# Optimization experiments

Measured on AMD Instinct MI355X. Metric: run time of the kernel, lower is better.

## Reference

```python
import jax, jax.numpy as jnp
import numpy as np

LN_EPS = 1e-5
BN_EPS = 1e-5
ALPHA = 0.1

def _layer_norm(x):
    # F.layer_norm over last dim, no affine
    mu = jnp.mean(x, axis=-1, keepdims=True)
    var = jnp.var(x, axis=-1, keepdims=True)
    return (x - mu) * jax.lax.rsqrt(var + LN_EPS)

def setup_inputs() -> dict:
    key = jax.random.key(0)
    ks = jax.random.split(key, 12)
    N, Nh, D, Dq = 8192, 8192, 64, 64
    s = 1.0 / np.sqrt(D)
    inp = {
        "X": jax.random.normal(ks[0], (N, D), jnp.float32),
        "H": jax.random.normal(ks[1], (Nh, D), jnp.float32),
        "M": jax.random.uniform(ks[2], (N, Nh), jnp.float32),
        # Linear params (torch nn.Linear: y = x @ W.T + b), uniform init scale
        "Qw": jax.random.uniform(ks[3], (Dq, D), jnp.float32, -s, s),
        "Qb": jax.random.uniform(ks[4], (Dq,), jnp.float32, -s, s),
        "Kw": jax.random.uniform(ks[5], (Dq, D), jnp.float32, -s, s),
        "Kb": jax.random.uniform(ks[6], (Dq,), jnp.float32, -s, s),
        "Vw": jax.random.uniform(ks[7], (64, D), jnp.float32, -s, s),
        "Vb": jax.random.uniform(ks[8], (64,), jnp.float32, -s, s),
        # BatchNorm1d(64) eval-mode params
        "bn_gamma": jnp.ones((64,), jnp.float32),
        "bn_beta": jnp.zeros((64,), jnp.float32),
        "bn_mean": 0.1 * jax.random.normal(ks[9], (64,), jnp.float32),
        "bn_var": jax.random.uniform(ks[10], (64,), jnp.float32, 0.5, 1.5),
    }
    return inp

def reference(X, H, M, Qw, Qb, Kw, Kb, Vw, Vb, bn_gamma, bn_beta, bn_mean, bn_var):
    # K/Q branches: Linear + LayerNorm
    K = _layer_norm(H @ Kw.T + Kb)            # [Nh, Dq]
    Q = _layer_norm(X @ Qw.T + Qb)            # [N, Dq]
    # V branch: Linear + BatchNorm1d (eval mode; dropout is identity in eval)
    V = (H @ Vw.T + Vb - bn_mean) * jax.lax.rsqrt(bn_var + BN_EPS) * bn_gamma + bn_beta  # [Nh, 64]
    # Masked attention, softmax over dim=0 (columns)
    A = (Q @ K.T) * 0.125                     # [N, Nh]
    A = jax.nn.softmax(M * A, axis=0)
    # globel=True branch
    return ALPHA * (A @ V) + M @ H            # [N, 64]
```

## Files before the change

kernel.cpp:

```cpp
#include <hip/hip_runtime.h>
#include <hip/hip_bf16.h>
#include <math.h>

#define NN 8192
#define QSCALE (0.125f * 1.44269504088896f)
#define OSZ (8192*64)

typedef __attribute__((ext_vector_type(8))) short short8;
typedef __attribute__((ext_vector_type(16))) float f32x16;
typedef __attribute__((ext_vector_type(4))) unsigned uint4e;
typedef __attribute__((ext_vector_type(2))) unsigned uint2e;

union W4 { uint4e u4; unsigned u[4]; short8 v; };

__device__ inline unsigned short f2bf(float x) {
  union { float f; unsigned u; } t; t.f = x;
  unsigned r = t.u + 0x7fffu + ((t.u >> 16) & 1u);
  return (unsigned short)(r >> 16);
}
__device__ inline unsigned cvtpk(float lo, float hi) {
  unsigned r;
  asm("v_cvt_pk_bf16_f32 %0, %1, %2" : "=v"(r) : "v"(lo), "v"(hi));
  return r;
}

__global__ __launch_bounds__(256) void qkv_kernel(
    const float* __restrict__ X, const float* __restrict__ H,
    const float* __restrict__ Qw, const float* __restrict__ Qb,
    const float* __restrict__ Kw, const float* __restrict__ Kb,
    const float* __restrict__ Vw, const float* __restrict__ Vb,
    const float* __restrict__ bng, const float* __restrict__ bnb,
    const float* __restrict__ bnm, const float* __restrict__ bnv,
    unsigned short* __restrict__ QP, unsigned short* __restrict__ KP,
    unsigned short* __restrict__ VP, unsigned short* __restrict__ HP)
{
  int wid = (blockIdx.x * blockDim.x + threadIdx.x) >> 6;
  int d = threadIdx.x & 63;
  float4 w[16];

  for (int fq = 0; fq < 16; fq++) w[fq] = *(const float4*)(Qw + d*64 + fq*4);
  for (int rr = 0; rr < 4; rr++) {
    int r = wid*4 + rr;
    float a = Qb[d];
    for (int fq = 0; fq < 16; fq++) {
      float4 xv = *(const float4*)(X + r*64 + fq*4);
      a += w[fq].x*xv.x + w[fq].y*xv.y + w[fq].z*xv.z + w[fq].w*xv.w;
    }
    float s = a;
    for (int off = 32; off; off >>= 1) s += __shfl_xor(s, off);
    float mean = s * (1.f/64.f);
    float c = a - mean;
    float s2 = c*c;
    for (int off = 32; off; off >>= 1) s2 += __shfl_xor(s2, off);
    float q = c * rsqrtf(s2*(1.f/64.f) + 1e-5f);
    QP[(d>>3)*65536 + r*8 + (d&7)] = f2bf(q * QSCALE);
  }
  for (int fq = 0; fq < 16; fq++) w[fq] = *(const float4*)(Kw + d*64 + fq*4);
  for (int rr = 0; rr < 4; rr++) {
    int r = wid*4 + rr;
    float a = Kb[d];
    for (int fq = 0; fq < 16; fq++) {
      float4 hv = *(const float4*)(H + r*64 + fq*4);
      a += w[fq].x*hv.x + w[fq].y*hv.y + w[fq].z*hv.z + w[fq].w*hv.w;
    }
    float s = a;
    for (int off = 32; off; off >>= 1) s += __shfl_xor(s, off);
    float mean = s * (1.f/64.f);
    float c = a - mean;
    float s2 = c*c;
    for (int off = 32; off; off >>= 1) s2 += __shfl_xor(s2, off);
    float k = c * rsqrtf(s2*(1.f/64.f) + 1e-5f);
    KP[(d>>3)*65536 + r*8 + (d&7)] = f2bf(k);
  }
  for (int fq = 0; fq < 16; fq++) w[fq] = *(const float4*)(Vw + d*64 + fq*4);
  float bscale = rsqrtf(bnv[d] + 1e-5f) * bng[d];
  for (int rr = 0; rr < 4; rr++) {
    int r = wid*4 + rr;
    float a = Vb[d];
    for (int fq = 0; fq < 16; fq++) {
      float4 hv = *(const float4*)(H + r*64 + fq*4);
      a += w[fq].x*hv.x + w[fq].y*hv.y + w[fq].z*hv.z + w[fq].w*hv.w;
    }
    float v = (a - bnm[d]) * bscale + bnb[d];
    VP[(r>>3)*512 + d*8 + (r&7)] = f2bf(v);
    HP[(r>>3)*512 + d*8 + (r&7)] = f2bf(H[r*64 + d]);
  }
}

__global__ __launch_bounds__(256) void pass1_kernel(
    const float* __restrict__ M, const unsigned short* __restrict__ QP,
    const unsigned short* __restrict__ KP, unsigned* __restrict__ MT4,
    float* __restrict__ pd)
{
  __shared__ __align__(16) float ld[4][32*34];
  int tid = threadIdx.x;
  int wj = (blockIdx.x * blockDim.x + tid) >> 6;
  int lane = tid & 63;
  int wv = tid >> 6;
  int l31 = lane & 31, h = lane >> 5;
  int jb = wj & 255, slice = wj >> 8;
  int j = jb*32 + l31;
  float* lds = ld[wv];

  short8 kb[4];
  for (int m = 0; m < 4; m++)
    kb[m] = *(const short8*)(KP + (2*m + h)*65536 + j*8);

  float d0 = 0.f, d1 = 0.f, d2 = 0.f, d3 = 0.f;
  for (int t = 0; t < 8; t++) {
    int i0 = (slice*8 + t) * 32;
    f32x16 acc;
    for (int r = 0; r < 16; r++) acc[r] = 0.f;
    for (int m = 0; m < 4; m++) {
      short8 qa = *(const short8*)(QP + (2*m + h)*65536 + (size_t)(i0 + l31)*8);
      acc = __builtin_amdgcn_mfma_f32_32x32x16_bf16(qa, kb[m], acc, 0, 0, 0);
    }
    float Mv[16];
#pragma unroll
    for (int r = 0; r < 16; r++) {
      int ir = (r&3) + 8*(r>>2) + 4*h;
      Mv[r] = __builtin_nontemporal_load(M + (size_t)(i0 + ir)*NN + j);
      lds[ir*34 + l31] = Mv[r];
    }
    d0 += exp2f(acc[0]*Mv[0]) + exp2f(acc[4]*Mv[4]) + exp2f(acc[8]*Mv[8])   + exp2f(acc[12]*Mv[12]);
    d1 += exp2f(acc[1]*Mv[1]) + exp2f(acc[5]*Mv[5]) + exp2f(acc[9]*Mv[9])   + exp2f(acc[13]*Mv[13]);
    d2 += exp2f(acc[2]*Mv[2]) + exp2f(acc[6]*Mv[6]) + exp2f(acc[10]*Mv[10]) + exp2f(acc[14]*Mv[14]);
    d3 += exp2f(acc[3]*Mv[3]) + exp2f(acc[7]*Mv[7]) + exp2f(acc[11]*Mv[11]) + exp2f(acc[15]*Mv[15]);

    asm volatile("s_waitcnt lgkmcnt(0)" ::: "memory");
    int ii = l31;
    int i_g = i0 + ii;
#pragma unroll
    for (int qq = 0; qq < 2; qq++) {
      int q = 2*h + qq;
      unsigned w0, w1, w2, w3;
      {
        float2 a2 = *(const float2*)(&lds[ii*34 + 8*q + 0]);
        float2 b2 = *(const float2*)(&lds[ii*34 + 8*q + 2]);
        float2 c2 = *(const float2*)(&lds[ii*34 + 8*q + 4]);
        float2 e2 = *(const float2*)(&lds[ii*34 + 8*q + 6]);
        w0 = cvtpk(a2.x, a2.y); w1 = cvtpk(b2.x, b2.y);
        w2 = cvtpk(c2.x, c2.y); w3 = cvtpk(e2.x, e2.y);
      }
      uint4e ww = {w0, w1, w2, w3};
      *(uint4e*)(MT4 + (size_t)(jb*4 + q)*32768 + (size_t)i_g*4) = ww;
    }
  }
  float drun = (d0 + d1) + (d2 + d3);
  drun += __shfl_xor(drun, 32);
  if (lane < 32) pd[(size_t)slice*NN + j] = drun;
}

__global__ __launch_bounds__(256) void combine_kernel(
    const float* __restrict__ pd, float* __restrict__ colcc)
{
  int j = blockIdx.x * blockDim.x + threadIdx.x;
  float Dv = 0.f;
  for (int s = 0; s < 32; s++) Dv += pd[(size_t)s*NN + j];
  colcc[j] = log2f(Dv * 10.f);
}

__global__ __launch_bounds__(256) void pass2_kernel(
    const unsigned* __restrict__ MT4, const unsigned short* __restrict__ QP,
    const unsigned short* __restrict__ KP, const unsigned short* __restrict__ VP,
    const unsigned short* __restrict__ HP, const float* __restrict__ colcc,
    float* __restrict__ opart)
{
  __shared__ __align__(16) float cls[512];

  int iblk = blockIdx.x >> 4, slice = blockIdx.x & 15;
  int i0 = iblk * 64;
  int tid = threadIdx.x;
  int lane = tid & 63, wid = tid >> 6;
  int l31 = lane & 31, h = lane >> 5;
  int iq = wid & 1, dh = wid >> 1;
  int row = iq*32 + l31;
  int i_g = i0 + row;

  short8 qb[4];
  for (int m = 0; m < 4; m++)
    qb[m] = *(const short8*)(QP + (2*m + h)*65536 + (size_t)i_g*8);

  cls[tid]       = colcc[slice*512 + tid];
  cls[tid + 256] = colcc[slice*512 + 256 + tid];
  __syncthreads();

  f32x16 oacc;
  for (int r = 0; r < 16; r++) oacc[r] = 0.f;

  const unsigned* mbase = MT4 + (size_t)i_g*4;

  for (int t = 0; t < 16; t++) {
    int jt = slice*512 + t*32;
    int jtb = jt >> 3;

    W4 A0, A1; uint2e E0, E1;
    A0.u4 = *(const uint4e*)(mbase + (size_t)(jtb + h)*32768);
    A1.u4 = *(const uint4e*)(mbase + (size_t)(jtb + 2 + h)*32768);
    E0    = *(const uint2e*)(mbase + (size_t)(jtb + (h ? 0 : 1))*32768 + 2*h);
    E1    = *(const uint2e*)(mbase + (size_t)(jtb + (h ? 2 : 3))*32768 + 2*h);

    f32x16 sacc;
    for (int r = 0; r < 16; r++) sacc[r] = 0.f;
    for (int m = 0; m < 4; m++) {
      short8 ka = *(const short8*)(KP + (2*m + h)*65536 + (size_t)(jt + l31)*8);
      sacc = __builtin_amdgcn_mfma_f32_32x32x16_bf16(ka, qb[m], sacc, 0, 0, 0);
    }

    unsigned mw[8];
    mw[0] = h ? E0.x    : A0.u[0];  mw[1] = h ? E0.y    : A0.u[1];
    mw[2] = h ? A0.u[2] : E0.x;     mw[3] = h ? A0.u[3] : E0.y;
    mw[4] = h ? E1.x    : A1.u[0];  mw[5] = h ? E1.y    : A1.u[1];
    mw[6] = h ? A1.u[2] : E1.x;     mw[7] = h ? A1.u[3] : E1.y;

    float p[16];
#pragma unroll
    for (int q = 0; q < 4; q++) {
      float4 cc = *(const float4*)(&cls[t*32 + 8*q + 4*h]);
      unsigned wa = mw[2*q], wb = mw[2*q + 1];
      float m0 = __uint_as_float(wa << 16);
      float m1 = __uint_as_float(wa & 0xffff0000u);
      float m2 = __uint_as_float(wb << 16);
      float m3 = __uint_as_float(wb & 0xffff0000u);
      p[4*q+0] = exp2f(fmaf(sacc[4*q+0], m0, -cc.x));
      p[4*q+1] = exp2f(fmaf(sacc[4*q+1], m1, -cc.y));
      p[4*q+2] = exp2f(fmaf(sacc[4*q+2], m2, -cc.z));
      p[4*q+3] = exp2f(fmaf(sacc[4*q+3], m3, -cc.w));
    }
    unsigned pu[8];
#pragma unroll
    for (int k = 0; k < 8; k++) pu[k] = cvtpk(p[2*k], p[2*k+1]);

    asm volatile("v_permlane32_swap_b32 %0, %1" : "+v"(pu[0]), "+v"(pu[2]));
    asm volatile("v_permlane32_swap_b32 %0, %1" : "+v"(pu[1]), "+v"(pu[3]));
    asm volatile("v_permlane32_swap_b32 %0, %1" : "+v"(pu[4]), "+v"(pu[6]));
    asm volatile("v_permlane32_swap_b32 %0, %1" : "+v"(pu[5]), "+v"(pu[7]));

    W4 PA0, PA1;
    PA0.u[0] = pu[0]; PA0.u[1] = pu[1]; PA0.u[2] = pu[2]; PA0.u[3] = pu[3];
    PA1.u[0] = pu[4]; PA1.u[1] = pu[5]; PA1.u[2] = pu[6]; PA1.u[3] = pu[7];

    int j8 = jt >> 3;
    const unsigned short* vbase = VP + (size_t)j8*512 + (dh*32 + l31)*8;
    const unsigned short* hbase = HP + (size_t)j8*512 + (dh*32 + l31)*8;
    short8 vb1 = *(const short8*)(vbase + h*512);
    short8 vb2 = *(const short8*)(vbase + (2 + h)*512);
    short8 hb1 = *(const short8*)(hbase + h*512);
    short8 hb2 = *(const short8*)(hbase + (2 + h)*512);

    oacc = __builtin_amdgcn_mfma_f32_32x32x16_bf16(PA0.v, vb1, oacc, 0, 0, 0);
    oacc = __builtin_amdgcn_mfma_f32_32x32x16_bf16(PA1.v, vb2, oacc, 0, 0, 0);
    oacc = __builtin_amdgcn_mfma_f32_32x32x16_bf16(A0.v,  hb1, oacc, 0, 0, 0);
    oacc = __builtin_amdgcn_mfma_f32_32x32x16_bf16(A1.v,  hb2, oacc, 0, 0, 0);
  }

  float* obase = opart + (size_t)slice*OSZ;
#pragma unroll
  for (int r = 0; r < 16; r++) {
    int orow = i0 + iq*32 + (r&3) + 8*(r>>2) + 4*h;
    int ocol = dh*32 + l31;
    obase[(size_t)orow*64 + ocol] = oacc[r];
  }
}

__global__ __launch_bounds__(256) void reduce_kernel(
    const float* __restrict__ opart, float* __restrict__ out)
{
  int e4 = blockIdx.x * blockDim.x + threadIdx.x;
  const float4* p = (const float4*)opart;
  float4 a = p[e4];
#pragma unroll
  for (int s = 1; s < 16; s++) {
    float4 b = p[(size_t)s*(OSZ/4) + e4];
    a.x += b.x; a.y += b.y; a.z += b.z; a.w += b.w;
  }
  ((float4*)out)[e4] = a;
}

extern "C" void kernel_launch(void* const* d_in, const int* in_sizes, int n_in,
                              void* d_out, int out_size, void* d_ws, size_t ws_size,
                              hipStream_t stream) {
  const float* X   = (const float*)d_in[0];
  const float* H   = (const float*)d_in[1];
  const float* M   = (const float*)d_in[2];
  const float* Qw  = (const float*)d_in[3];
  const float* Qb  = (const float*)d_in[4];
  const float* Kw  = (const float*)d_in[5];
  const float* Kb  = (const float*)d_in[6];
  const float* Vw  = (const float*)d_in[7];
  const float* Vb  = (const float*)d_in[8];
  const float* bng = (const float*)d_in[9];
  const float* bnb = (const float*)d_in[10];
  const float* bnm = (const float*)d_in[11];
  const float* bnv = (const float*)d_in[12];
  float* out = (float*)d_out;

  char* ws = (char*)d_ws;
  const size_t MB = 1024*1024;
  unsigned* MT4       = (unsigned*)(ws);
  unsigned short* QP  = (unsigned short*)(ws + 128*MB);
  unsigned short* KP  = (unsigned short*)(ws + 129*MB);
  unsigned short* VP  = (unsigned short*)(ws + 130*MB);
  unsigned short* HP  = (unsigned short*)(ws + 131*MB);
  float* pd           = (float*)(ws + 132*MB);
  float* colcc        = (float*)(ws + 133*MB);
  float* opart        = (float*)(ws + 134*MB);

  qkv_kernel<<<512, 256, 0, stream>>>(X, H, Qw, Qb, Kw, Kb, Vw, Vb,
                                      bng, bnb, bnm, bnv, QP, KP, VP, HP);
  pass1_kernel<<<2048, 256, 0, stream>>>(M, QP, KP, MT4, pd);
  combine_kernel<<<32, 256, 0, stream>>>(pd, colcc);
  pass2_kernel<<<2048, 256, 0, stream>>>(MT4, QP, KP, VP, HP, colcc, opart);
  reduce_kernel<<<512, 256, 0, stream>>>(opart, out);
}
```

Before: 200.7 us.

## Prefetch next-tile M and K loads; derive mask words via permlane swap

In pass1, the M tile for the next row block is loaded one iteration early into registers so its global load latency overlaps the current MFMA and exp work. In pass2, the next tile's transposed-mask words and K fragments are software-prefetched, and V/H fragment loads are moved to the top of the loop. The two extra uint2 mask loads are replaced by v_permlane32_swap on the already-loaded words. This costs extra registers, which could lower occupancy. There is also a leftover redundant assignment (A0c = A1n) that is immediately overwritten.

```diff
diff --git a/kernel.cpp b/kernel.cpp
--- a/kernel.cpp
+++ b/kernel.cpp
@@ -9,7 +9,6 @@
 typedef __attribute__((ext_vector_type(8))) short short8;
 typedef __attribute__((ext_vector_type(16))) float f32x16;
 typedef __attribute__((ext_vector_type(4))) unsigned uint4e;
-typedef __attribute__((ext_vector_type(2))) unsigned uint2e;
 
 union W4 { uint4e u4; unsigned u[4]; short8 v; };
 
@@ -106,20 +105,39 @@
   for (int m = 0; m < 4; m++)
     kb[m] = *(const short8*)(KP + (2*m + h)*65536 + j*8);
 
+  float Mv[16];
+  {
+    int i0 = slice*8*32;
+#pragma unroll
+    for (int r = 0; r < 16; r++) {
+      int ir = (r&3) + 8*(r>>2) + 4*h;
+      Mv[r] = __builtin_nontemporal_load(M + (size_t)(i0 + ir)*NN + j);
+    }
+  }
+
   float d0 = 0.f, d1 = 0.f, d2 = 0.f, d3 = 0.f;
   for (int t = 0; t < 8; t++) {
     int i0 = (slice*8 + t) * 32;
+    float Mn[16];
+    if (t < 7) {
+      int i1 = i0 + 32;
+#pragma unroll
+      for (int r = 0; r < 16; r++) {
+        int ir = (r&3) + 8*(r>>2) + 4*h;
+        Mn[r] = __builtin_nontemporal_load(M + (size_t)(i1 + ir)*NN + j);
+      }
+    }
+
     f32x16 acc;
     for (int r = 0; r < 16; r++) acc[r] = 0.f;
     for (int m = 0; m < 4; m++) {
       short8 qa = *(const short8*)(QP + (2*m + h)*65536 + (size_t)(i0 + l31)*8);
       acc = __builtin_amdgcn_mfma_f32_32x32x16_bf16(qa, kb[m], acc, 0, 0, 0);
     }
-    float Mv[16];
+
 #pragma unroll
     for (int r = 0; r < 16; r++) {
       int ir = (r&3) + 8*(r>>2) + 4*h;
-      Mv[r] = __builtin_nontemporal_load(M + (size_t)(i0 + ir)*NN + j);
       lds[ir*34 + l31] = Mv[r];
     }
     d0 += exp2f(acc[0]*Mv[0]) + exp2f(acc[4]*Mv[4]) + exp2f(acc[8]*Mv[8])   + exp2f(acc[12]*Mv[12]);
@@ -145,6 +163,10 @@
       uint4e ww = {w0, w1, w2, w3};
       *(uint4e*)(MT4 + (size_t)(jb*4 + q)*32768 + (size_t)i_g*4) = ww;
     }
+    if (t < 7) {
+#pragma unroll
+      for (int r = 0; r < 16; r++) Mv[r] = Mn[r];
+    }
   }
   float drun = (d0 + d1) + (d2 + d3);
   drun += __shfl_xor(drun, 32);
@@ -190,28 +212,49 @@
 
   const unsigned* mbase = MT4 + (size_t)i_g*4;
 
+  W4 A0c, A1c; short8 kac[4];
+  {
+    int jt = slice*512, jtb = jt >> 3;
+    A0c.u4 = *(const uint4e*)(mbase + (size_t)(jtb + h)*32768);
+    A1c.u4 = *(const uint4e*)(mbase + (size_t)(jtb + 2 + h)*32768);
+    for (int m = 0; m < 4; m++)
+      kac[m] = *(const short8*)(KP + (2*m + h)*65536 + (size_t)(jt + l31)*8);
+  }
+
   for (int t = 0; t < 16; t++) {
     int jt = slice*512 + t*32;
-    int jtb = jt >> 3;
-
-    W4 A0, A1; uint2e E0, E1;
-    A0.u4 = *(const uint4e*)(mbase + (size_t)(jtb + h)*32768);
-    A1.u4 = *(const uint4e*)(mbase + (size_t)(jtb + 2 + h)*32768);
-    E0    = *(const uint2e*)(mbase + (size_t)(jtb + (h ? 0 : 1))*32768 + 2*h);
-    E1    = *(const uint2e*)(mbase + (size_t)(jtb + (h ? 2 : 3))*32768 + 2*h);
+
+    W4 A0n, A1n; short8 kan[4];
+    if (t < 15) {
+      int jn = jt + 32, jnb = jn >> 3;
+      A0n.u4 = *(const uint4e*)(mbase + (size_t)(jnb + h)*32768);
+      A1n.u4 = *(const uint4e*)(mbase + (size_t)(jnb + 2 + h)*32768);
+      for (int m = 0; m < 4; m++)
+        kan[m] = *(const short8*)(KP + (2*m + h)*65536 + (size_t)(jn + l31)*8);
+    }
+
+    int j8 = jt >> 3;
+    const unsigned short* vbase = VP + (size_t)j8*512 + (dh*32 + l31)*8;
+    const unsigned short* hbase = HP + (size_t)j8*512 + (dh*32 + l31)*8;
+    short8 vb1 = *(const short8*)(vbase + h*512);
+    short8 vb2 = *(const short8*)(vbase + (2 + h)*512);
+    short8 hb1 = *(const short8*)(hbase + h*512);
+    short8 hb2 = *(const short8*)(hbase + (2 + h)*512);
 
     f32x16 sacc;
     for (int r = 0; r < 16; r++) sacc[r] = 0.f;
-    for (int m = 0; m < 4; m++) {
-      short8 ka = *(const short8*)(KP + (2*m + h)*65536 + (size_t)(jt + l31)*8);
-      sacc = __builtin_amdgcn_mfma_f32_32x32x16_bf16(ka, qb[m], sacc, 0, 0, 0);
-    }
-
-    unsigned mw[8];
-    mw[0] = h ? E0.x    : A0.u[0];  mw[1] = h ? E0.y    : A0.u[1];
-    mw[2] = h ? A0.u[2] : E0.x;     mw[3] = h ? A0.u[3] : E0.y;
-    mw[4] = h ? E1.x    : A1.u[0];  mw[5] = h ? E1.y    : A1.u[1];
-    mw[6] = h ? A1.u[2] : E1.x;     mw[7] = h ? A1.u[3] : E1.y;
+    for (int m = 0; m < 4; m++)
+      sacc = __builtin_amdgcn_mfma_f32_32x32x16_bf16(kac[m], qb[m], sacc, 0, 0, 0);
+
+    unsigned mw0 = A0c.u[0], mw2 = A0c.u[2];
+    unsigned mw1 = A0c.u[1], mw3 = A0c.u[3];
+    unsigned mw4 = A1c.u[0], mw6 = A1c.u[2];
+    unsigned mw5 = A1c.u[1], mw7 = A1c.u[3];
+    asm volatile("v_permlane32_swap_b32 %0, %1" : "+v"(mw0), "+v"(mw2));
+    asm volatile("v_permlane32_swap_b32 %0, %1" : "+v"(mw1), "+v"(mw3));
+    asm volatile("v_permlane32_swap_b32 %0, %1" : "+v"(mw4), "+v"(mw6));
+    asm volatile("v_permlane32_swap_b32 %0, %1" : "+v"(mw5), "+v"(mw7));
+    unsigned mw[8] = {mw0, mw1, mw2, mw3, mw4, mw5, mw6, mw7};
 
     float p[16];
 #pragma unroll
@@ -240,18 +283,18 @@
     PA0.u[0] = pu[0]; PA0.u[1] = pu[1]; PA0.u[2] = pu[2]; PA0.u[3] = pu[3];
     PA1.u[0] = pu[4]; PA1.u[1] = pu[5]; PA1.u[2] = pu[6]; PA1.u[3] = pu[7];
 
-    int j8 = jt >> 3;
-    const unsigned short* vbase = VP + (size_t)j8*512 + (dh*32 + l31)*8;
-    const unsigned short* hbase = HP + (size_t)j8*512 + (dh*32 + l31)*8;
-    short8 vb1 = *(const short8*)(vbase + h*512);
-    short8 vb2 = *(const short8*)(vbase + (2 + h)*512);
-    short8 hb1 = *(const short8*)(hbase + h*512);
-    short8 hb2 = *(const short8*)(hbase + (2 + h)*512);
-
     oacc = __builtin_amdgcn_mfma_f32_32x32x16_bf16(PA0.v, vb1, oacc, 0, 0, 0);
     oacc = __builtin_amdgcn_mfma_f32_32x32x16_bf16(PA1.v, vb2, oacc, 0, 0, 0);
-    oacc = __builtin_amdgcn_mfma_f32_32x32x16_bf16(A0.v,  hb1, oacc, 0, 0, 0);
-    oacc = __builtin_amdgcn_mfma_f32_32x32x16_bf16(A1.v,  hb2, oacc, 0, 0, 0);
+    oacc = __builtin_amdgcn_mfma_f32_32x32x16_bf16(A0c.v, hb1, oacc, 0, 0, 0);
+    oacc = __builtin_amdgcn_mfma_f32_32x32x16_bf16(A1c.v, hb2, oacc, 0, 0, 0);
+
+    if (t < 15) {
+      A0c = A1n;
+    }
+    if (t < 15) {
+      A0c = A0n; A1c = A1n;
+      for (int m = 0; m < 4; m++) kac[m] = kan[m];
+    }
   }
 
   float* obase = opart + (size_t)slice*OSZ;
```

Measured after the change: 200.8 us. No clear change (+0.1%).

## Drop bf16 transposed M copy; re-read fp32 M in pass2 via LDS

Applied to the files above, without the earlier changes.

Pass1 no longer writes a transposed bf16 copy of M (128MB workspace). It now only computes column denominators, prefetching the next M tile into registers and using raw v_exp_f32. Pass2 instead streams fp32 M directly through double-buffered LDS tiles, converting to bf16 in registers with permlane swaps, and uses 8 slices instead of 16, which halves the partial-output reduction. This trades a 128MB write plus 128MB bf16 read for a second 256MB fp32 read of M, and adds LDS traffic and per-tile barriers.

```diff
diff --git a/kernel.cpp b/kernel.cpp
--- a/kernel.cpp
+++ b/kernel.cpp
@@ -5,13 +5,12 @@
 #define NN 8192
 #define QSCALE (0.125f * 1.44269504088896f)
 #define OSZ (8192*64)
+#define NSL 8
 
 typedef __attribute__((ext_vector_type(8))) short short8;
 typedef __attribute__((ext_vector_type(16))) float f32x16;
-typedef __attribute__((ext_vector_type(4))) unsigned uint4e;
-typedef __attribute__((ext_vector_type(2))) unsigned uint2e;
-
-union W4 { uint4e u4; unsigned u[4]; short8 v; };
+
+union W4 { unsigned u[4]; short8 v; };
 
 __device__ inline unsigned short f2bf(float x) {
   union { float f; unsigned u; } t; t.f = x;
@@ -21,6 +20,11 @@
 __device__ inline unsigned cvtpk(float lo, float hi) {
   unsigned r;
   asm("v_cvt_pk_bf16_f32 %0, %1, %2" : "=v"(r) : "v"(lo), "v"(hi));
+  return r;
+}
+__device__ inline float fexp2(float x) {
+  float r;
+  asm("v_exp_f32 %0, %1" : "=v"(r) : "v"(x));
   return r;
 }
 
@@ -89,61 +93,57 @@
 
 __global__ __launch_bounds__(256) void pass1_kernel(
     const float* __restrict__ M, const unsigned short* __restrict__ QP,
-    const unsigned short* __restrict__ KP, unsigned* __restrict__ MT4,
-    float* __restrict__ pd)
-{
-  __shared__ __align__(16) float ld[4][32*34];
+    const unsigned short* __restrict__ KP, float* __restrict__ pd)
+{
   int tid = threadIdx.x;
   int wj = (blockIdx.x * blockDim.x + tid) >> 6;
   int lane = tid & 63;
-  int wv = tid >> 6;
   int l31 = lane & 31, h = lane >> 5;
   int jb = wj & 255, slice = wj >> 8;
   int j = jb*32 + l31;
-  float* lds = ld[wv];
 
   short8 kb[4];
   for (int m = 0; m < 4; m++)
     kb[m] = *(const short8*)(KP + (2*m + h)*65536 + j*8);
 
+  float Mv[16];
+  {
+    int i0 = slice*8*32;
+#pragma unroll
+    for (int r = 0; r < 16; r++) {
+      int ir = (r&3) + 8*(r>>2) + 4*h;
+      Mv[r] = __builtin_nontemporal_load(M + (size_t)(i0 + ir)*NN + j);
+    }
+  }
+
   float d0 = 0.f, d1 = 0.f, d2 = 0.f, d3 = 0.f;
   for (int t = 0; t < 8; t++) {
     int i0 = (slice*8 + t) * 32;
+    float Mn[16];
+    if (t < 7) {
+      int i1 = i0 + 32;
+#pragma unroll
+      for (int r = 0; r < 16; r++) {
+        int ir = (r&3) + 8*(r>>2) + 4*h;
+        Mn[r] = __builtin_nontemporal_load(M + (size_t)(i1 + ir)*NN + j);
+      }
+    }
+
     f32x16 acc;
     for (int r = 0; r < 16; r++) acc[r] = 0.f;
     for (int m = 0; m < 4; m++) {
       short8 qa = *(const short8*)(QP + (2*m + h)*65536 + (size_t)(i0 + l31)*8);
       acc = __builtin_amdgcn_mfma_f32_32x32x16_bf16(qa, kb[m], acc, 0, 0, 0);
     }
-    float Mv[16];
-#pragma unroll
-    for (int r = 0; r < 16; r++) {
-      int ir = (r&3) + 8*(r>>2) + 4*h;
-      Mv[r] = __builtin_nontemporal_load(M + (size_t)(i0 + ir)*NN + j);
-      lds[ir*34 + l31] = Mv[r];
-    }
-    d0 += exp2f(acc[0]*Mv[0]) + exp2f(acc[4]*Mv[4]) + exp2f(acc[8]*Mv[8])   + exp2f(acc[12]*Mv[12]);
-    d1 += exp2f(acc[1]*Mv[1]) + exp2f(acc[5]*Mv[5]) + exp2f(acc[9]*Mv[9])   + exp2f(acc[13]*Mv[13]);
-    d2 += exp2f(acc[2]*Mv[2]) + exp2f(acc[6]*Mv[6]) + exp2f(acc[10]*Mv[10]) + exp2f(acc[14]*Mv[14]);
-    d3 += exp2f(acc[3]*Mv[3]) + exp2f(acc[7]*Mv[7]) + exp2f(acc[11]*Mv[11]) + exp2f(acc[15]*Mv[15]);
-
-    asm volatile("s_waitcnt lgkmcnt(0)" ::: "memory");
-    int ii = l31;
-    int i_g = i0 + ii;
-#pragma unroll
-    for (int qq = 0; qq < 2; qq++) {
-      int q = 2*h + qq;
-      unsigned w0, w1, w2, w3;
-      {
-        float2 a2 = *(const float2*)(&lds[ii*34 + 8*q + 0]);
-        float2 b2 = *(const float2*)(&lds[ii*34 + 8*q + 2]);
-        float2 c2 = *(const float2*)(&lds[ii*34 + 8*q + 4]);
-        float2 e2 = *(const float2*)(&lds[ii*34 + 8*q + 6]);
-        w0 = cvtpk(a2.x, a2.y); w1 = cvtpk(b2.x, b2.y);
-        w2 = cvtpk(c2.x, c2.y); w3 = cvtpk(e2.x, e2.y);
-      }
-      uint4e ww = {w0, w1, w2, w3};
-      *(uint4e*)(MT4 + (size_t)(jb*4 + q)*32768 + (size_t)i_g*4) = ww;
+
+    d0 += fexp2(acc[0]*Mv[0]) + fexp2(acc[4]*Mv[4]) + fexp2(acc[8]*Mv[8])   + fexp2(acc[12]*Mv[12]);
+    d1 += fexp2(acc[1]*Mv[1]) + fexp2(acc[5]*Mv[5]) + fexp2(acc[9]*Mv[9])   + fexp2(acc[13]*Mv[13]);
+    d2 += fexp2(acc[2]*Mv[2]) + fexp2(acc[6]*Mv[6]) + fexp2(acc[10]*Mv[10]) + fexp2(acc[14]*Mv[14]);
+    d3 += fexp2(acc[3]*Mv[3]) + fexp2(acc[7]*Mv[7]) + fexp2(acc[11]*Mv[11]) + fexp2(acc[15]*Mv[15]);
+
+    if (t < 7) {
+#pragma unroll
+      for (int r = 0; r < 16; r++) Mv[r] = Mn[r];
     }
   }
   float drun = (d0 + d1) + (d2 + d3);
@@ -160,15 +160,18 @@
   colcc[j] = log2f(Dv * 10.f);
 }
 
+#define MST 66
+
 __global__ __launch_bounds__(256) void pass2_kernel(
-    const unsigned* __restrict__ MT4, const unsigned short* __restrict__ QP,
+    const float* __restrict__ M, const unsigned short* __restrict__ QP,
     const unsigned short* __restrict__ KP, const unsigned short* __restrict__ VP,
     const unsigned short* __restrict__ HP, const float* __restrict__ colcc,
     float* __restrict__ opart)
 {
-  __shared__ __align__(16) float cls[512];
-
-  int iblk = blockIdx.x >> 4, slice = blockIdx.x & 15;
+  __shared__ __align__(16) float mt[2][64*MST];
+  __shared__ __align__(16) float cls[1024];
+
+  int iblk = blockIdx.x >> 3, slice = blockIdx.x & 7;
   int i0 = iblk * 64;
   int tid = threadIdx.x;
   int lane = tid & 63, wid = tid >> 6;
@@ -181,77 +184,105 @@
   for (int m = 0; m < 4; m++)
     qb[m] = *(const short8*)(QP + (2*m + h)*65536 + (size_t)i_g*8);
 
-  cls[tid]       = colcc[slice*512 + tid];
-  cls[tid + 256] = colcc[slice*512 + 256 + tid];
+#pragma unroll
+  for (int k = 0; k < 4; k++)
+    cls[tid + k*256] = colcc[slice*1024 + k*256 + tid];
+
+  const float* msrc = M + (size_t)i0*NN + slice*1024;
+
+#pragma unroll
+  for (int q = 0; q < 4; q++) {
+    int idx = q*256 + tid, r = idx >> 4, c = (idx & 15) * 4;
+    float4 v = *(const float4*)(msrc + (size_t)r*NN + c);
+    float* dst = &mt[0][r*MST + c];
+    *(float2*)(dst)     = make_float2(v.x, v.y);
+    *(float2*)(dst + 2) = make_float2(v.z, v.w);
+  }
   __syncthreads();
 
   f32x16 oacc;
   for (int r = 0; r < 16; r++) oacc[r] = 0.f;
 
-  const unsigned* mbase = MT4 + (size_t)i_g*4;
-
-  for (int t = 0; t < 16; t++) {
-    int jt = slice*512 + t*32;
-    int jtb = jt >> 3;
-
-    W4 A0, A1; uint2e E0, E1;
-    A0.u4 = *(const uint4e*)(mbase + (size_t)(jtb + h)*32768);
-    A1.u4 = *(const uint4e*)(mbase + (size_t)(jtb + 2 + h)*32768);
-    E0    = *(const uint2e*)(mbase + (size_t)(jtb + (h ? 0 : 1))*32768 + 2*h);
-    E1    = *(const uint2e*)(mbase + (size_t)(jtb + (h ? 2 : 3))*32768 + 2*h);
-
-    f32x16 sacc;
-    for (int r = 0; r < 16; r++) sacc[r] = 0.f;
-    for (int m = 0; m < 4; m++) {
-      short8 ka = *(const short8*)(KP + (2*m + h)*65536 + (size_t)(jt + l31)*8);
-      sacc = __builtin_amdgcn_mfma_f32_32x32x16_bf16(ka, qb[m], sacc, 0, 0, 0);
-    }
-
-    unsigned mw[8];
-    mw[0] = h ? E0.x    : A0.u[0];  mw[1] = h ? E0.y    : A0.u[1];
-    mw[2] = h ? A0.u[2] : E0.x;     mw[3] = h ? A0.u[3] : E0.y;
-    mw[4] = h ? E1.x    : A1.u[0];  mw[5] = h ? E1.y    : A1.u[1];
-    mw[6] = h ? A1.u[2] : E1.x;     mw[7] = h ? A1.u[3] : E1.y;
-
-    float p[16];
-#pragma unroll
-    for (int q = 0; q < 4; q++) {
-      float4 cc = *(const float4*)(&cls[t*32 + 8*q + 4*h]);
-      unsigned wa = mw[2*q], wb = mw[2*q + 1];
-      float m0 = __uint_as_float(wa << 16);
-      float m1 = __uint_as_float(wa & 0xffff0000u);
-      float m2 = __uint_as_float(wb << 16);
-      float m3 = __uint_as_float(wb & 0xffff0000u);
-      p[4*q+0] = exp2f(fmaf(sacc[4*q+0], m0, -cc.x));
-      p[4*q+1] = exp2f(fmaf(sacc[4*q+1], m1, -cc.y));
-      p[4*q+2] = exp2f(fmaf(sacc[4*q+2], m2, -cc.z));
-      p[4*q+3] = exp2f(fmaf(sacc[4*q+3], m3, -cc.w));
-    }
-    unsigned pu[8];
-#pragma unroll
-    for (int k = 0; k < 8; k++) pu[k] = cvtpk(p[2*k], p[2*k+1]);
-
-    asm volatile("v_permlane32_swap_b32 %0, %1" : "+v"(pu[0]), "+v"(pu[2]));
-    asm volatile("v_permlane32_swap_b32 %0, %1" : "+v"(pu[1]), "+v"(pu[3]));
-    asm volatile("v_permlane32_swap_b32 %0, %1" : "+v"(pu[4]), "+v"(pu[6]));
-    asm volatile("v_permlane32_swap_b32 %0, %1" : "+v"(pu[5]), "+v"(pu[7]));
-
-    W4 PA0, PA1;
-    PA0.u[0] = pu[0]; PA0.u[1] = pu[1]; PA0.u[2] = pu[2]; PA0.u[3] = pu[3];
-    PA1.u[0] = pu[4]; PA1.u[1] = pu[5]; PA1.u[2] = pu[6]; PA1.u[3] = pu[7];
-
-    int j8 = jt >> 3;
-    const unsigned short* vbase = VP + (size_t)j8*512 + (dh*32 + l31)*8;
-    const unsigned short* hbase = HP + (size_t)j8*512 + (dh*32 + l31)*8;
-    short8 vb1 = *(const short8*)(vbase + h*512);
-    short8 vb2 = *(const short8*)(vbase + (2 + h)*512);
-    short8 hb1 = *(const short8*)(hbase + h*512);
-    short8 hb2 = *(const short8*)(hbase + (2 + h)*512);
-
-    oacc = __builtin_amdgcn_mfma_f32_32x32x16_bf16(PA0.v, vb1, oacc, 0, 0, 0);
-    oacc = __builtin_amdgcn_mfma_f32_32x32x16_bf16(PA1.v, vb2, oacc, 0, 0, 0);
-    oacc = __builtin_amdgcn_mfma_f32_32x32x16_bf16(A0.v,  hb1, oacc, 0, 0, 0);
-    oacc = __builtin_amdgcn_mfma_f32_32x32x16_bf16(A1.v,  hb2, oacc, 0, 0, 0);
+  for (int tm = 0; tm < 16; tm++) {
+    if (tm < 15) {
+      const float* src = msrc + (tm+1)*64;
+      float* dstb = mt[(tm+1) & 1];
+#pragma unroll
+      for (int q = 0; q < 4; q++) {
+        int idx = q*256 + tid, r = idx >> 4, c = (idx & 15) * 4;
+        float4 v = *(const float4*)(src + (size_t)r*NN + c);
+        float* dst = &dstb[r*MST + c];
+        *(float2*)(dst)     = make_float2(v.x, v.y);
+        *(float2*)(dst + 2) = make_float2(v.z, v.w);
+      }
+    }
+    const float* mb = mt[tm & 1];
+
+#pragma unroll
+    for (int ti = 0; ti < 2; ti++) {
+      int jt = slice*1024 + tm*64 + ti*32;
+      int jloc = tm*64 + ti*32;
+
+      f32x16 sacc;
+      for (int r = 0; r < 16; r++) sacc[r] = 0.f;
+      for (int m = 0; m < 4; m++) {
+        short8 ka = *(const short8*)(KP + (2*m + h)*65536 + (size_t)(jt + l31)*8);
+        sacc = __builtin_amdgcn_mfma_f32_32x32x16_bf16(ka, qb[m], sacc, 0, 0, 0);
+      }
+
+      float2 mv2[8];
+#pragma unroll
+      for (int q = 0; q < 4; q++) {
+        const float* rb = &mb[row*MST + ti*32 + 8*q + 4*h];
+        mv2[2*q]   = *(const float2*)(rb);
+        mv2[2*q+1] = *(const float2*)(rb + 2);
+      }
+
+      float p[16];
+#pragma unroll
+      for (int q = 0; q < 4; q++) {
+        float4 cc = *(const float4*)(&cls[jloc + 8*q + 4*h]);
+        p[4*q+0] = fexp2(fmaf(sacc[4*q+0], mv2[2*q].x,   -cc.x));
+        p[4*q+1] = fexp2(fmaf(sacc[4*q+1], mv2[2*q].y,   -cc.y));
+        p[4*q+2] = fexp2(fmaf(sacc[4*q+2], mv2[2*q+1].x, -cc.z));
+        p[4*q+3] = fexp2(fmaf(sacc[4*q+3], mv2[2*q+1].y, -cc.w));
+      }
+
+      unsigned pu[8], mw[8];
+#pragma unroll
+      for (int k = 0; k < 8; k++) pu[k] = cvtpk(p[2*k], p[2*k+1]);
+#pragma unroll
+      for (int k = 0; k < 8; k++) mw[k] = cvtpk(mv2[k].x, mv2[k].y);
+
+      asm volatile("v_permlane32_swap_b32 %0, %1" : "+v"(pu[0]), "+v"(pu[2]));
+      asm volatile("v_permlane32_swap_b32 %0, %1" : "+v"(pu[1]), "+v"(pu[3]));
+      asm volatile("v_permlane32_swap_b32 %0, %1" : "+v"(pu[4]), "+v"(pu[6]));
+      asm volatile("v_permlane32_swap_b32 %0, %1" : "+v"(pu[5]), "+v"(pu[7]));
+      asm volatile("v_permlane32_swap_b32 %0, %1" : "+v"(mw[0]), "+v"(mw[2]));
+      asm volatile("v_permlane32_swap_b32 %0, %1" : "+v"(mw[1]), "+v"(mw[3]));
+      asm volatile("v_permlane32_swap_b32 %0, %1" : "+v"(mw[4]), "+v"(mw[6]));
+      asm volatile("v_permlane32_swap_b32 %0, %1" : "+v"(mw[5]), "+v"(mw[7]));
+
+      W4 PA0, PA1, MA0, MA1;
+      PA0.u[0] = pu[0]; PA0.u[1] = pu[1]; PA0.u[2] = pu[2]; PA0.u[3] = pu[3];
+      PA1.u[0] = pu[4]; PA1.u[1] = pu[5]; PA1.u[2] = pu[6]; PA1.u[3] = pu[7];
+      MA0.u[0] = mw[0]; MA0.u[1] = mw[1]; MA0.u[2] = mw[2]; MA0.u[3] = mw[3];
+      MA1.u[0] = mw[4]; MA1.u[1] = mw[5]; MA1.u[2] = mw[6]; MA1.u[3] = mw[7];
+
+      int j8 = jt >> 3;
+      const unsigned short* vbase = VP + (size_t)j8*512 + (dh*32 + l31)*8;
+      const unsigned short* hbase = HP + (size_t)j8*512 + (dh*32 + l31)*8;
+      short8 vb1 = *(const short8*)(vbase + h*512);
+      short8 vb2 = *(const short8*)(vbase + (2 + h)*512);
+      short8 hb1 = *(const short8*)(hbase + h*512);
+      short8 hb2 = *(const short8*)(hbase + (2 + h)*512);
+
+      oacc = __builtin_amdgcn_mfma_f32_32x32x16_bf16(PA0.v, vb1, oacc, 0, 0, 0);
+      oacc = __builtin_amdgcn_mfma_f32_32x32x16_bf16(PA1.v, vb2, oacc, 0, 0, 0);
+      oacc = __builtin_amdgcn_mfma_f32_32x32x16_bf16(MA0.v, hb1, oacc, 0, 0, 0);
+      oacc = __builtin_amdgcn_mfma_f32_32x32x16_bf16(MA1.v, hb2, oacc, 0, 0, 0);
+    }
+    __syncthreads();
   }
 
   float* obase = opart + (size_t)slice*OSZ;
@@ -270,7 +301,7 @@
   const float4* p = (const float4*)opart;
   float4 a = p[e4];
 #pragma unroll
-  for (int s = 1; s < 16; s++) {
+  for (int s = 1; s < NSL; s++) {
     float4 b = p[(size_t)s*(OSZ/4) + e4];
     a.x += b.x; a.y += b.y; a.z += b.z; a.w += b.w;
   }
@@ -297,19 +328,18 @@
 
   char* ws = (char*)d_ws;
   const size_t MB = 1024*1024;
-  unsigned* MT4       = (unsigned*)(ws);
-  unsigned short* QP  = (unsigned short*)(ws + 128*MB);
-  unsigned short* KP  = (unsigned short*)(ws + 129*MB);
-  unsigned short* VP  = (unsigned short*)(ws + 130*MB);
-  unsigned short* HP  = (unsigned short*)(ws + 131*MB);
-  float* pd           = (float*)(ws + 132*MB);
-  float* colcc        = (float*)(ws + 133*MB);
-  float* opart        = (float*)(ws + 134*MB);
+  unsigned short* QP  = (unsigned short*)(ws);
+  unsigned short* KP  = (unsigned short*)(ws + 1*MB);
+  unsigned short* VP  = (unsigned short*)(ws + 2*MB);
+  unsigned short* HP  = (unsigned short*)(ws + 3*MB);
+  float* pd           = (float*)(ws + 4*MB);
+  float* colcc        = (float*)(ws + 5*MB);
+  float* opart        = (float*)(ws + 6*MB);
 
   qkv_kernel<<<512, 256, 0, stream>>>(X, H, Qw, Qb, Kw, Kb, Vw, Vb,
                                       bng, bnb, bnm, bnv, QP, KP, VP, HP);
-  pass1_kernel<<<2048, 256, 0, stream>>>(M, QP, KP, MT4, pd);
+  pass1_kernel<<<2048, 256, 0, stream>>>(M, QP, KP, pd);
   combine_kernel<<<32, 256, 0, stream>>>(pd, colcc);
-  pass2_kernel<<<2048, 256, 0, stream>>>(MT4, QP, KP, VP, HP, colcc, opart);
+  pass2_kernel<<<1024, 256, 0, stream>>>(M, QP, KP, VP, HP, colcc, opart);
   reduce_kernel<<<512, 256, 0, stream>>>(opart, out);
 }
```

Result: slower. 235.7 us (+17.4%).
